# Kernel tuning notes

Measured on AMD Instinct MI355X. Metric: run time of the kernel, lower is better.

## Reference

```python
import jax, jax.numpy as jnp
import numpy as np
import math

D_MODEL = 1024
N_HEADS = 16
D_HEAD = D_MODEL // N_HEADS
D_FF = 4096
BATCH = 2
SEQ = 2048
EPS = 1e-5


def _rmsnorm(x, w):
    rms = jnp.sqrt(jnp.mean(x * x, axis=-1, keepdims=True) + EPS)
    return (x / rms) * w


def _gelu_erf(x):
    # matches 0.5 * x * (1 + erf(x / sqrt(2)))
    return 0.5 * x * (1.0 + jax.lax.erf(x / jnp.sqrt(jnp.asarray(2.0, x.dtype))))


def setup_inputs() -> dict:
    key = jax.random.key(0)
    ks = jax.random.split(key, 6)
    scale = 0.02
    x = jax.random.normal(ks[0], (BATCH, SEQ, D_MODEL), dtype=jnp.float32)
    w_qkv = jax.random.normal(ks[1], (3 * D_MODEL, D_MODEL), dtype=jnp.float32) * scale
    w_o = jax.random.normal(ks[2], (D_MODEL, D_MODEL), dtype=jnp.float32) * scale
    ln1_w = jnp.ones((D_MODEL,), dtype=jnp.float32)
    ln2_w = jnp.ones((D_MODEL,), dtype=jnp.float32)
    w1 = jax.random.normal(ks[3], (D_FF, D_MODEL), dtype=jnp.float32) * scale
    w2 = jax.random.normal(ks[4], (D_MODEL, D_FF), dtype=jnp.float32) * scale
    return {"x": x, "w_qkv": w_qkv, "w_o": w_o, "ln1_w": ln1_w,
            "ln2_w": ln2_w, "w1": w1, "w2": w2}


def reference(x, w_qkv, w_o, ln1_w, ln2_w, w1, w2):
    B, S, D = x.shape
    # --- attention sublayer (pre-norm) ---
    h = _rmsnorm(x, ln1_w)
    qkv = jnp.einsum('bsd,ed->bse', h, w_qkv)            # (B,S,3*D)
    qkv = qkv.reshape(B, S, 3, N_HEADS, D_HEAD)
    q, k, v = jnp.moveaxis(qkv, 2, 0)                    # each (B,S,H,dh)
    q = q.transpose(0, 2, 1, 3)                          # (B,H,S,dh)
    k = k.transpose(0, 2, 1, 3)
    v = v.transpose(0, 2, 1, 3)
    scores = jnp.einsum('bhqd,bhkd->bhqk', q, k) / math.sqrt(D_HEAD)
    causal = jnp.tril(jnp.ones((S, S), dtype=bool))      # True = keep
    scores = jnp.where(causal, scores, jnp.asarray(-jnp.inf, scores.dtype))
    attn = jax.nn.softmax(scores, axis=-1)
    ctx = jnp.einsum('bhqk,bhkd->bhqd', attn, v)         # (B,H,S,dh)
    ctx = ctx.transpose(0, 2, 1, 3).reshape(B, S, D)
    attn_out = jnp.einsum('bsd,ed->bse', ctx, w_o)
    first_sum = x + attn_out
    # --- FFN sublayer (pre-norm) ---
    h2 = _rmsnorm(first_sum, ln2_w)
    ff = jnp.einsum('bsf,df->bsd', _gelu_erf(jnp.einsum('bsd,fd->bsf', h2, w1)), w2)
    return first_sum + ff
```

## Files before the change

kernel.cpp:

```cpp
#include <hip/hip_runtime.h>

typedef unsigned short u16;
typedef unsigned int u32;
typedef __attribute__((ext_vector_type(8))) short short8;
typedef __attribute__((ext_vector_type(4))) float f32x4;

#define AS1 __attribute__((address_space(1)))
#define AS3 __attribute__((address_space(3)))

__device__ __forceinline__ u16 f2bf(float f) {
  union { float f; unsigned u; } v; v.f = f;
  return (u16)((v.u + 0x7fffu + ((v.u >> 16) & 1u)) >> 16);
}
__device__ __forceinline__ u32 pack2bf(float a, float b) {
  return (u32)f2bf(a) | ((u32)f2bf(b) << 16);
}
__device__ __forceinline__ u32 permpack(float a, float b) {
  union { float f; u32 u; } ua, ub; ua.f = a; ub.f = b;
  return __builtin_amdgcn_perm(ub.u, ua.u, 0x07060302u);
}

__global__ void cvt_kernel(const float* __restrict__ in, u16* __restrict__ out,
                           float scale) {
  int i = (blockIdx.x * 256 + threadIdx.x) * 4;
  float4 v = *(const float4*)(in + i);
  ushort4 o = make_ushort4(f2bf(v.x * scale), f2bf(v.y * scale),
                           f2bf(v.z * scale), f2bf(v.w * scale));
  *(ushort4*)(out + i) = o;
}

__global__ void rmsnorm_kernel(const float* __restrict__ x, const float* __restrict__ w,
                               u16* __restrict__ out) {
  const int row = blockIdx.x, tid = threadIdx.x;
  const float4 v = ((const float4*)(x + (size_t)row * 1024))[tid];
  float ss = v.x * v.x + v.y * v.y + v.z * v.z + v.w * v.w;
#pragma unroll
  for (int off = 32; off > 0; off >>= 1) ss += __shfl_xor(ss, off);
  __shared__ float red[4];
  if ((tid & 63) == 0) red[tid >> 6] = ss;
  __syncthreads();
  float tot = red[0] + red[1] + red[2] + red[3];
  float scale = 1.0f / sqrtf(tot * (1.0f / 1024.0f) + 1e-5f);
  const float4 wv = ((const float4*)w)[tid];
  ushort4 o = make_ushort4(f2bf(v.x * scale * wv.x), f2bf(v.y * scale * wv.y),
                           f2bf(v.z * scale * wv.z), f2bf(v.w * scale * wv.w));
  ((ushort4*)(out + (size_t)row * 1024))[tid] = o;
}

template <int EPI>
__global__ __launch_bounds__(256)
void gemm_bt(const u16* __restrict__ A, const u16* __restrict__ B,
             const float* __restrict__ RES, void* __restrict__ OUT,
             int M, int N, int K, int KS) {
  __shared__ __align__(16) u16 As[128 * 32];
  __shared__ __align__(16) u16 Bs[128 * 32];
  const int tid = threadIdx.x;
  const int wave = tid >> 6, lane = tid & 63;
  const int quad = lane >> 4, l16 = lane & 15;
  const int m0 = blockIdx.y * 128, n0 = blockIdx.x * 128;
  const int wm = (wave >> 1) * 64, wn = (wave & 1) * 64;
  f32x4 acc[4][4] = {};

  const int c0 = wave * 128 + lane;
  const int r0_row = c0 >> 2, r0_col = ((c0 & 3) ^ (r0_row & 3)) * 8;
  const int c1 = c0 + 64;
  const int r1_row = c1 >> 2, r1_col = ((c1 & 3) ^ (r1_row & 3)) * 8;

  const int kbeg = blockIdx.z * KS, kend = kbeg + KS;
  for (int k0 = kbeg; k0 < kend; k0 += 32) {
    __syncthreads();
    {
      u16* ga0 = (u16*)(A + (size_t)(m0 + r0_row) * K + k0 + r0_col);
      u16* ga1 = (u16*)(A + (size_t)(m0 + r1_row) * K + k0 + r1_col);
      u16* gb0 = (u16*)(B + (size_t)(n0 + r0_row) * K + k0 + r0_col);
      u16* gb1 = (u16*)(B + (size_t)(n0 + r1_row) * K + k0 + r1_col);
      __builtin_amdgcn_global_load_lds((AS1 void*)ga0, (AS3 void*)(As + wave * 1024), 16, 0, 0);
      __builtin_amdgcn_global_load_lds((AS1 void*)ga1, (AS3 void*)(As + wave * 1024 + 512), 16, 0, 0);
      __builtin_amdgcn_global_load_lds((AS1 void*)gb0, (AS3 void*)(Bs + wave * 1024), 16, 0, 0);
      __builtin_amdgcn_global_load_lds((AS1 void*)gb1, (AS3 void*)(Bs + wave * 1024 + 512), 16, 0, 0);
    }
    __syncthreads();
    const int rcol = (quad ^ (l16 & 3)) * 8;
    short8 af[4], bfr[4];
#pragma unroll
    for (int i = 0; i < 4; ++i) {
      af[i]  = *(const short8*)(As + (wm + i * 16 + l16) * 32 + rcol);
      bfr[i] = *(const short8*)(Bs + (wn + i * 16 + l16) * 32 + rcol);
    }
#pragma unroll
    for (int i = 0; i < 4; ++i)
#pragma unroll
      for (int j = 0; j < 4; ++j)
        acc[i][j] = __builtin_amdgcn_mfma_f32_16x16x32_bf16(af[i], bfr[j], acc[i][j], 0, 0, 0);
  }

  const size_t zoff = (size_t)blockIdx.z * M * N;
#pragma unroll
  for (int i = 0; i < 4; ++i) {
#pragma unroll
    for (int j = 0; j < 4; ++j) {
#pragma unroll
      for (int r = 0; r < 4; ++r) {
        int row = m0 + wm + i * 16 + quad * 4 + r;
        int col = n0 + wn + j * 16 + l16;
        size_t idx = (size_t)row * N + col;
        float v = acc[i][j][r];
        if constexpr (EPI == 0) {
          ((u16*)OUT)[idx] = f2bf(v);
        } else if constexpr (EPI == 1) {
          ((float*)OUT)[idx] = RES[idx] + v;
        } else if constexpr (EPI == 2) {
          float g = 0.5f * v * (1.0f + erff(v * 0.70710678118654752f));
          ((u16*)OUT)[idx] = f2bf(g);
        } else {
          ((float*)OUT)[zoff + idx] = v;
        }
      }
    }
  }
}

__global__ void reduce4_kernel(const float* __restrict__ fs,
                               const float* __restrict__ P,
                               float* __restrict__ out, size_t n) {
  size_t i = ((size_t)blockIdx.x * 256 + threadIdx.x) * 4;
  float4 a = *(const float4*)(fs + i);
  float4 p0 = *(const float4*)(P + i);
  float4 p1 = *(const float4*)(P + n + i);
  float4 p2 = *(const float4*)(P + 2 * n + i);
  float4 p3 = *(const float4*)(P + 3 * n + i);
  float4 o = make_float4(a.x + ((p0.x + p1.x) + (p2.x + p3.x)),
                         a.y + ((p0.y + p1.y) + (p2.y + p3.y)),
                         a.z + ((p0.z + p1.z) + (p2.z + p3.z)),
                         a.w + ((p0.w + p1.w) + (p2.w + p3.w)));
  *(float4*)(out + i) = o;
}

__global__ __launch_bounds__(256)
void packkv_kernel(const u16* __restrict__ qkv, u16* __restrict__ Kp,
                   u16* __restrict__ Vp) {
  __shared__ __align__(16) u16 Ks[32][72];
  __shared__ __align__(16) u16 Vs[32][72];
  const int kt = blockIdx.x, h = blockIdx.y, b = blockIdx.z;
  const int tid = threadIdx.x;
  const int key0 = kt * 32;
  {
    const size_t g = (size_t)b * 2048 * 3072 + (size_t)(key0 + (tid >> 3)) * 3072
                     + h * 64 + (tid & 7) * 8;
    *(short8*)(&Ks[tid >> 3][(tid & 7) * 8]) = *(const short8*)(qkv + g + 1024);
    *(short8*)(&Vs[tid >> 3][(tid & 7) * 8]) = *(const short8*)(qkv + g + 2048);
  }
  __syncthreads();
  const int wave = tid >> 6, lane = tid & 63;
  const int quad = lane >> 4, l16 = lane & 15;
  const int permrow = 8 * (l16 >> 2) + (l16 & 3);
  const size_t obase = ((size_t)((b * 16 + h) * 64 + kt)) * 2048 + tid * 8;
  {
    int row = permrow + (wave >> 1) * 4;
    int col = quad * 8 + (wave & 1) * 32;
    *(short8*)(Kp + obase) = *(const short8*)(&Ks[row][col]);
  }
  {
    short8 v;
    int col = wave * 16 + l16;
#pragma unroll
    for (int j = 0; j < 8; ++j) v[j] = (short)Vs[quad * 8 + j][col];
    *(short8*)(Vp + obase) = v;
  }
}

struct AttnState {
  f32x4 o0, o1, o2, o3;
  float ls;
};

template <bool MASKED>
__device__ __forceinline__ void attn_tile(
    AttnState& st, const u16* kp, const u16* vp, int key0, int q_abs, int quad,
    short8 qf0, short8 qf1) {
  short8 kf00 = *(const short8*)kp;
  short8 kf01 = *(const short8*)(kp + 512);
  short8 kf10 = *(const short8*)(kp + 1024);
  short8 kf11 = *(const short8*)(kp + 1536);
  short8 vf0 = *(const short8*)vp;
  short8 vf1 = *(const short8*)(vp + 512);
  short8 vf2 = *(const short8*)(vp + 1024);
  short8 vf3 = *(const short8*)(vp + 1536);

  f32x4 s0 = {}, s1 = {};
  s0 = __builtin_amdgcn_mfma_f32_16x16x32_bf16(kf00, qf0, s0, 0, 0, 0);
  s0 = __builtin_amdgcn_mfma_f32_16x16x32_bf16(kf01, qf1, s0, 0, 0, 0);
  s1 = __builtin_amdgcn_mfma_f32_16x16x32_bf16(kf10, qf0, s1, 0, 0, 0);
  s1 = __builtin_amdgcn_mfma_f32_16x16x32_bf16(kf11, qf1, s1, 0, 0, 0);

  float p[8];
#pragma unroll
  for (int r = 0; r < 4; ++r) {
    p[r]     = __expf(s0[r]);
    p[4 + r] = __expf(s1[r]);
  }
  if constexpr (MASKED) {
    const int kb = key0 + 8 * quad;
#pragma unroll
    for (int r = 0; r < 4; ++r) {
      if (kb + r > q_abs)     p[r] = 0.f;
      if (kb + 4 + r > q_abs) p[4 + r] = 0.f;
    }
  }
  st.ls += ((p[0] + p[1]) + (p[2] + p[3])) + ((p[4] + p[5]) + (p[6] + p[7]));

  union { u32 u[4]; short8 s; } pu;
  pu.u[0] = permpack(p[0], p[1]);
  pu.u[1] = permpack(p[2], p[3]);
  pu.u[2] = permpack(p[4], p[5]);
  pu.u[3] = permpack(p[6], p[7]);

  st.o0 = __builtin_amdgcn_mfma_f32_16x16x32_bf16(vf0, pu.s, st.o0, 0, 0, 0);
  st.o1 = __builtin_amdgcn_mfma_f32_16x16x32_bf16(vf1, pu.s, st.o1, 0, 0, 0);
  st.o2 = __builtin_amdgcn_mfma_f32_16x16x32_bf16(vf2, pu.s, st.o2, 0, 0, 0);
  st.o3 = __builtin_amdgcn_mfma_f32_16x16x32_bf16(vf3, pu.s, st.o3, 0, 0, 0);
}

__global__ __launch_bounds__(256)
void attn_kernel(const u16* __restrict__ qkv, const u16* __restrict__ Kpack,
                 const u16* __restrict__ Vpack, u16* __restrict__ ctx) {
  const int bx = blockIdx.x, by = blockIdx.y, bz = blockIdx.z;
  const int h = by, b = bz;
  const int qt = ((by >> 3) & 1) ? (31 - bx) : bx;
  const int tid = threadIdx.x, wave = tid >> 6, lane = tid & 63;
  const int quad = lane >> 4, l16 = lane & 15;
  const int q0 = qt * 64;
  const int qrow = q0 + wave * 16;
  const int q_abs = qrow + l16;
  const size_t base = (size_t)b * 2048 * 3072;
  const size_t headoff = (size_t)((b * 16 + h) * 64) * 2048;
  const u16* Kb = Kpack + headoff + lane * 8;
  const u16* Vb = Vpack + headoff + lane * 8;

  short8 qf0, qf1;
  {
    const u16* qp = qkv + base + (size_t)q_abs * 3072 + h * 64 + quad * 8;
    qf0 = *(const short8*)qp;
    qf1 = *(const short8*)(qp + 32);
  }
  AttnState st;
  st.o0 = f32x4{}; st.o1 = f32x4{}; st.o2 = f32x4{}; st.o3 = f32x4{};
  st.ls = 0.f;

  const int nfull = qrow >> 5;
  for (int kt = 0; kt < nfull; ++kt)
    attn_tile<false>(st, Kb + kt * 2048, Vb + kt * 2048, kt * 32, q_abs, quad, qf0, qf1);
  attn_tile<true>(st, Kb + nfull * 2048, Vb + nfull * 2048, nfull * 32, q_abs, quad, qf0, qf1);

  float ls = st.ls;
  ls += __shfl_xor(ls, 16);
  ls += __shfl_xor(ls, 32);
  float inv = 1.0f / ls;

  f32x4 o[4] = {st.o0, st.o1, st.o2, st.o3};
  u16* cp = ctx + (size_t)(b * 2048 + q_abs) * 1024 + h * 64 + quad * 4;
#pragma unroll
  for (int c = 0; c < 4; ++c) {
    u32 lo = pack2bf(o[c][0] * inv, o[c][1] * inv);
    u32 hi = pack2bf(o[c][2] * inv, o[c][3] * inv);
    *(uint2*)(cp + c * 16) = make_uint2(lo, hi);
  }
}

extern "C" void kernel_launch(void* const* d_in, const int* in_sizes, int n_in,
                              void* d_out, int out_size, void* d_ws, size_t ws_size,
                              hipStream_t stream) {
  const float* x     = (const float*)d_in[0];
  const float* w_qkv = (const float*)d_in[1];
  const float* w_o   = (const float*)d_in[2];
  const float* ln1   = (const float*)d_in[3];
  const float* ln2   = (const float*)d_in[4];
  const float* w1    = (const float*)d_in[5];
  const float* w2    = (const float*)d_in[6];
  float* out = (float*)d_out;

  char* p = (char*)d_ws;
  u16* wqkv_b = (u16*)p; p += (size_t)3072 * 1024 * 2;
  u16* wo_b   = (u16*)p; p += (size_t)1024 * 1024 * 2;
  u16* w1_b   = (u16*)p; p += (size_t)4096 * 1024 * 2;
  u16* w2_b   = (u16*)p; p += (size_t)1024 * 4096 * 2;
  u16* h_b    = (u16*)p; p += (size_t)4096 * 1024 * 2;
  u16* qkv_b  = (u16*)p;
  u16* g_b    = qkv_b;
  p += (size_t)4096 * 3072 * 2;
  u16* ctx_b  = (u16*)p; p += (size_t)4096 * 1024 * 2;
  float* fs   = (float*)p; p += (size_t)4096 * 1024 * 4;
  u16* kp_b   = (u16*)fs;
  u16* vp_b   = (u16*)fs + (size_t)4 * 1024 * 1024;
  float* Pbuf = (float*)p;
  const size_t need = (size_t)(p - (char*)d_ws) + (size_t)4 * 4096 * 1024 * 4;
  const bool splitk = ws_size >= need;

  cvt_kernel<<<1024, 256, 0, stream>>>(w_qkv, wqkv_b, 1.0f);
  cvt_kernel<<<1024, 256, 0, stream>>>(w_qkv + 1024 * 1024, wqkv_b + 1024 * 1024, 0.125f);
  cvt_kernel<<<1024, 256, 0, stream>>>(w_qkv + 2 * 1024 * 1024, wqkv_b + 2 * 1024 * 1024, 1.0f);
  cvt_kernel<<<1024, 256, 0, stream>>>(w_o, wo_b, 1.0f);
  cvt_kernel<<<4096, 256, 0, stream>>>(w1, w1_b, 1.0f);
  cvt_kernel<<<4096, 256, 0, stream>>>(w2, w2_b, 1.0f);

  rmsnorm_kernel<<<4096, 256, 0, stream>>>(x, ln1, h_b);
  gemm_bt<0><<<dim3(24, 32, 1), 256, 0, stream>>>(h_b, wqkv_b, nullptr, qkv_b, 4096, 3072, 1024, 1024);
  packkv_kernel<<<dim3(64, 16, 2), 256, 0, stream>>>(qkv_b, kp_b, vp_b);
  attn_kernel<<<dim3(32, 16, 2), 256, 0, stream>>>(qkv_b, kp_b, vp_b, ctx_b);
  gemm_bt<1><<<dim3(8, 32, 1), 256, 0, stream>>>(ctx_b, wo_b, x, fs, 4096, 1024, 1024, 1024);
  rmsnorm_kernel<<<4096, 256, 0, stream>>>(fs, ln2, h_b);
  gemm_bt<2><<<dim3(32, 32, 1), 256, 0, stream>>>(h_b, w1_b, nullptr, g_b, 4096, 4096, 1024, 1024);
  if (splitk) {
    gemm_bt<3><<<dim3(8, 32, 4), 256, 0, stream>>>(g_b, w2_b, nullptr, Pbuf, 4096, 1024, 4096, 1024);
    reduce4_kernel<<<4096, 256, 0, stream>>>(fs, Pbuf, out, (size_t)4096 * 1024);
  } else {
    gemm_bt<1><<<dim3(8, 32, 1), 256, 0, stream>>>(g_b, w2_b, fs, out, 4096, 1024, 4096, 4096);
  }
}
```

Baseline: 390.5 us.

## Double GEMM K-step to 64 with fragment-native LDS layout; fuse weight conversions

```diff
diff --git a/kernel.cpp b/kernel.cpp
--- a/kernel.cpp
+++ b/kernel.cpp
@@ -20,13 +20,27 @@
   return __builtin_amdgcn_perm(ub.u, ua.u, 0x07060302u);
 }
 
-__global__ void cvt_kernel(const float* __restrict__ in, u16* __restrict__ out,
-                           float scale) {
-  int i = (blockIdx.x * 256 + threadIdx.x) * 4;
-  float4 v = *(const float4*)(in + i);
+__global__ void cvt_all_kernel(const float* __restrict__ wqkv, const float* __restrict__ wo,
+                               const float* __restrict__ w1, const float* __restrict__ w2,
+                               u16* __restrict__ oqkv, u16* __restrict__ oo,
+                               u16* __restrict__ o1, u16* __restrict__ o2) {
+  const int blk = blockIdx.x;
+  const float* src; u16* dst; float scale = 1.0f; int off;
+  if (blk < 3072) {
+    src = wqkv; dst = oqkv; off = blk;
+    if (blk >= 1024 && blk < 2048) scale = 0.125f;
+  } else if (blk < 4096) {
+    src = wo; dst = oo; off = blk - 3072;
+  } else if (blk < 8192) {
+    src = w1; dst = o1; off = blk - 4096;
+  } else {
+    src = w2; dst = o2; off = blk - 8192;
+  }
+  size_t i = ((size_t)off * 256 + threadIdx.x) * 4;
+  float4 v = *(const float4*)(src + i);
   ushort4 o = make_ushort4(f2bf(v.x * scale), f2bf(v.y * scale),
                            f2bf(v.z * scale), f2bf(v.w * scale));
-  *(ushort4*)(out + i) = o;
+  *(ushort4*)(dst + i) = o;
 }
 
 __global__ void rmsnorm_kernel(const float* __restrict__ x, const float* __restrict__ w,
@@ -52,8 +66,8 @@
 void gemm_bt(const u16* __restrict__ A, const u16* __restrict__ B,
              const float* __restrict__ RES, void* __restrict__ OUT,
              int M, int N, int K, int KS) {
-  __shared__ __align__(16) u16 As[128 * 32];
-  __shared__ __align__(16) u16 Bs[128 * 32];
+  __shared__ __align__(16) u16 As[16 * 512];
+  __shared__ __align__(16) u16 Bs[16 * 512];
   const int tid = threadIdx.x;
   const int wave = tid >> 6, lane = tid & 63;
   const int quad = lane >> 4, l16 = lane & 15;
@@ -61,37 +75,47 @@
   const int wm = (wave >> 1) * 64, wn = (wave & 1) * 64;
   f32x4 acc[4][4] = {};
 
-  const int c0 = wave * 128 + lane;
-  const int r0_row = c0 >> 2, r0_col = ((c0 & 3) ^ (r0_row & 3)) * 8;
-  const int c1 = c0 + 64;
-  const int r1_row = c1 >> 2, r1_col = ((c1 & 3) ^ (r1_row & 3)) * 8;
+  const int g0 = 2 * wave;
+  const int arow0 = m0 + 16 * g0 + l16;
+  const int brow0 = n0 + 16 * g0 + l16;
+  const int kcol = quad * 8;
+  u16* asl = As + g0 * 1024;
+  u16* bsl = Bs + g0 * 1024;
 
   const int kbeg = blockIdx.z * KS, kend = kbeg + KS;
-  for (int k0 = kbeg; k0 < kend; k0 += 32) {
+  for (int k0 = kbeg; k0 < kend; k0 += 64) {
     __syncthreads();
     {
-      u16* ga0 = (u16*)(A + (size_t)(m0 + r0_row) * K + k0 + r0_col);
-      u16* ga1 = (u16*)(A + (size_t)(m0 + r1_row) * K + k0 + r1_col);
-      u16* gb0 = (u16*)(B + (size_t)(n0 + r0_row) * K + k0 + r0_col);
-      u16* gb1 = (u16*)(B + (size_t)(n0 + r1_row) * K + k0 + r1_col);
-      __builtin_amdgcn_global_load_lds((AS1 void*)ga0, (AS3 void*)(As + wave * 1024), 16, 0, 0);
-      __builtin_amdgcn_global_load_lds((AS1 void*)ga1, (AS3 void*)(As + wave * 1024 + 512), 16, 0, 0);
-      __builtin_amdgcn_global_load_lds((AS1 void*)gb0, (AS3 void*)(Bs + wave * 1024), 16, 0, 0);
-      __builtin_amdgcn_global_load_lds((AS1 void*)gb1, (AS3 void*)(Bs + wave * 1024 + 512), 16, 0, 0);
+      const u16* a0 = A + (size_t)arow0 * K + k0 + kcol;
+      const u16* a1 = a0 + (size_t)16 * K;
+      const u16* b0 = B + (size_t)brow0 * K + k0 + kcol;
+      const u16* b1 = b0 + (size_t)16 * K;
+      __builtin_amdgcn_global_load_lds((AS1 void*)a0, (AS3 void*)(asl), 16, 0, 0);
+      __builtin_amdgcn_global_load_lds((AS1 void*)(a0 + 32), (AS3 void*)(asl + 512), 16, 0, 0);
+      __builtin_amdgcn_global_load_lds((AS1 void*)a1, (AS3 void*)(asl + 1024), 16, 0, 0);
+      __builtin_amdgcn_global_load_lds((AS1 void*)(a1 + 32), (AS3 void*)(asl + 1536), 16, 0, 0);
+      __builtin_amdgcn_global_load_lds((AS1 void*)b0, (AS3 void*)(bsl), 16, 0, 0);
+      __builtin_amdgcn_global_load_lds((AS1 void*)(b0 + 32), (AS3 void*)(bsl + 512), 16, 0, 0);
+      __builtin_amdgcn_global_load_lds((AS1 void*)b1, (AS3 void*)(bsl + 1024), 16, 0, 0);
+      __builtin_amdgcn_global_load_lds((AS1 void*)(b1 + 32), (AS3 void*)(bsl + 1536), 16, 0, 0);
     }
     __syncthreads();
-    const int rcol = (quad ^ (l16 & 3)) * 8;
-    short8 af[4], bfr[4];
-#pragma unroll
-    for (int i = 0; i < 4; ++i) {
-      af[i]  = *(const short8*)(As + (wm + i * 16 + l16) * 32 + rcol);
-      bfr[i] = *(const short8*)(Bs + (wn + i * 16 + l16) * 32 + rcol);
+    const u16* ar = As + (wm >> 4) * 1024 + lane * 8;
+    const u16* br = Bs + (wn >> 4) * 1024 + lane * 8;
+#pragma unroll
+    for (int kk = 0; kk < 2; ++kk) {
+      short8 af[4], bfr[4];
+#pragma unroll
+      for (int i = 0; i < 4; ++i) {
+        af[i]  = *(const short8*)(ar + i * 1024 + kk * 512);
+        bfr[i] = *(const short8*)(br + i * 1024 + kk * 512);
+      }
+#pragma unroll
+      for (int i = 0; i < 4; ++i)
+#pragma unroll
+        for (int j = 0; j < 4; ++j)
+          acc[i][j] = __builtin_amdgcn_mfma_f32_16x16x32_bf16(af[i], bfr[j], acc[i][j], 0, 0, 0);
     }
-#pragma unroll
-    for (int i = 0; i < 4; ++i)
-#pragma unroll
-      for (int j = 0; j < 4; ++j)
-        acc[i][j] = __builtin_amdgcn_mfma_f32_16x16x32_bf16(af[i], bfr[j], acc[i][j], 0, 0, 0);
   }
 
   const size_t zoff = (size_t)blockIdx.z * M * N;
@@ -296,12 +320,8 @@
   const size_t need = (size_t)(p - (char*)d_ws) + (size_t)4 * 4096 * 1024 * 4;
   const bool splitk = ws_size >= need;
 
-  cvt_kernel<<<1024, 256, 0, stream>>>(w_qkv, wqkv_b, 1.0f);
-  cvt_kernel<<<1024, 256, 0, stream>>>(w_qkv + 1024 * 1024, wqkv_b + 1024 * 1024, 0.125f);
-  cvt_kernel<<<1024, 256, 0, stream>>>(w_qkv + 2 * 1024 * 1024, wqkv_b + 2 * 1024 * 1024, 1.0f);
-  cvt_kernel<<<1024, 256, 0, stream>>>(w_o, wo_b, 1.0f);
-  cvt_kernel<<<4096, 256, 0, stream>>>(w1, w1_b, 1.0f);
-  cvt_kernel<<<4096, 256, 0, stream>>>(w2, w2_b, 1.0f);
+  cvt_all_kernel<<<12288, 256, 0, stream>>>(w_qkv, w_o, w1, w2,
+                                            wqkv_b, wo_b, w1_b, w2_b);
 
   rmsnorm_kernel<<<4096, 256, 0, stream>>>(x, ln1, h_b);
   gemm_bt<0><<<dim3(24, 32, 1), 256, 0, stream>>>(h_b, wqkv_b, nullptr, qkv_b, 4096, 3072, 1024, 1024);
```

Measured after the change: 427.7 us. 9.5% more time.
